# Kernel optimization log

Measured on AMD Instinct MI355X. Metric: run time of the kernel, lower is better.

The kernel has to match this reference:

```python
import jax, jax.numpy as jnp
import numpy as np

D1 = 3          # elevated lattice dim (self.d == self.d1 == 3 in source)
S = 384         # size2d = 128*3
B, N = 32, 65536

# canonical simplex offsets, built exactly as in __init__
_c = np.tile(np.arange(D1), (D1, 1))
for _i in range(1, D1):
    _c[-_i:, _i] = _i - D1
CANONICAL = jnp.asarray(_c, dtype=jnp.int32)  # [[0,1,2],[0,1,-1],[0,-2,-1]]


def setup_inputs() -> dict:
    key = jax.random.key(0)
    k1, k2, k3 = jax.random.split(key, 3)
    # get_model.scalePoints rescales coords to ~0.8*size2d; emulate that range
    pc1 = jax.random.uniform(k1, (B, 3, N), dtype=jnp.float32) * (0.8 * S)
    features = jax.random.normal(k2, (B, 3, N), dtype=jnp.float32)
    tm = jax.random.normal(k3, (B, 3, 3), dtype=jnp.float32)
    # F.normalize(trans_matrix, dim=1)
    trans_mat = tm / jnp.maximum(jnp.linalg.norm(tm, axis=1, keepdims=True), 1e-12)
    return {"pc1": pc1, "features": features, "trans_mat": trans_mat}


def _keys_and_barycentric(pc, trans_mat):
    b, _, n = pc.shape
    elevated = jnp.einsum('bij,bjn->bin', trans_mat, pc)          # (B,3,N)
    greedy = jnp.round(elevated / D1) * D1
    emg = elevated - greedy
    # rank = inverse permutation of descending argsort over the 3 lattice dims
    order = jnp.argsort(-emg, axis=1)
    rank = jnp.argsort(order, axis=1).astype(jnp.int32)           # (B,3,N)
    rs = jnp.sum(greedy, axis=1, keepdims=True) / D1              # (B,1,N)
    rf = rank.astype(jnp.float32)
    cond = (((rf >= D1 - rs) & (rs > 0)) | ((rf < -rs) & (rs < 0))).astype(jnp.float32)
    sign = jnp.where(rs > 0, -1.0, 0.0) + jnp.where(rs < 0, 1.0, 0.0)
    greedy = greedy + D1 * sign * cond
    rank = rank + (D1 * sign * cond).astype(jnp.int32)
    rank = rank + rs.astype(jnp.int32)
    emg2 = elevated - greedy
    greedy_i = greedy.astype(jnp.int32)
    b_ix = jnp.arange(b)[:, None, None]
    n_ix = jnp.arange(n)[None, None, :]
    # NOTE: source uses self.d - rank for += and self.d1 - rank for -=, but d==d1,
    # so the two scatter-adds cancel exactly; barycentric degenerates to [1,0,0].
    # Reproduce the same computation faithfully.
    bary = jnp.zeros((b, D1 + 1, n), jnp.float32)
    bary = bary.at[b_ix, D1 - rank, n_ix].add(emg2)
    bary = bary.at[b_ix, D1 - rank, n_ix].add(-emg2)
    bary = bary / D1
    bary = bary.at[:, 0, :].add(1.0 + bary[:, D1, :])
    bary = bary[:, :D1, :]                                        # (B,3,N)
    keys = greedy_i[:, :, :, None] + CANONICAL[rank]              # (B,3,N,3)
    return keys, bary


def reference(pc1, features, trans_mat):
    keys, bary = _keys_and_barycentric(pc1, trans_mat)
    b = features.shape[0]
    coord = keys[:, :2].reshape(b, 2, -1)                          # (B,2,3N)
    offset = coord.min(axis=2)                                     # (B,2) int
    coord = coord - offset[:, :, None]
    # tmp[b, n*3+j, c] = bary[b, j, n] * features[b, c, n]
    tmp = bary[:, None, :, :] * features[:, :, None, :]            # (B,3,3,N)
    tmp = jnp.transpose(tmp, (0, 1, 3, 2)).reshape(b, 3, -1)       # (B,3,3N)
    tmp = jnp.transpose(tmp, (0, 2, 1))                            # (B,3N,3)
    pts_pick = (-offset) % D1                                      # (B,2)
    oob = coord >= S
    coord = jnp.where(oob, 0, coord)
    bad = jnp.sum(oob, axis=1) > 0                                 # (B,3N)
    tmp = jnp.where(bad[:, :, None], 0.0, tmp)

    ar = jnp.arange(S // D1)

    def splat_one(cd, vals, pick):
        sp = jnp.zeros((S, S, 3), jnp.float32).at[cd[0], cd[1]].add(vals)
        return sp[pick[0] + D1 * ar][:, pick[1] + D1 * ar]

    filter_2d = jax.vmap(splat_one)(coord, tmp, pts_pick)          # (B,S/3,S/3,3)
    return filter_2d
```

## Files before the change

### kernel.cpp

```cpp
#include <hip/hip_runtime.h>
#include <stdint.h>

#define NPTS 65536
#define NB   32
#define SS   384

#define C3INV 0.333333343267440796f

#define FP_SCALE 32768.0f
#define FP_INV   (1.0f / 32768.0f)

__device__ __forceinline__ float fmul_strict(float a, float b) {
    float r;
    asm volatile("v_mul_f32 %0, %1, %2" : "=v"(r) : "v"(a), "v"(b));
    return r;
}
__device__ __forceinline__ float fadd_strict(float a, float b) {
    float r;
    asm volatile("v_add_f32 %0, %1, %2" : "=v"(r) : "v"(a), "v"(b));
    return r;
}

__device__ __forceinline__ void lattice_point(
    const float* __restrict__ t,
    float p0, float p1, float p2,
    int& gi0, int& gi1, int& rc0, int& rc1)
{
    float e0 = fadd_strict(fadd_strict(fmul_strict(t[0], p0), fmul_strict(t[1], p1)), fmul_strict(t[2], p2));
    float e1 = fadd_strict(fadd_strict(fmul_strict(t[3], p0), fmul_strict(t[4], p1)), fmul_strict(t[5], p2));
    float e2 = fadd_strict(fadd_strict(fmul_strict(t[6], p0), fmul_strict(t[7], p1)), fmul_strict(t[8], p2));

    float g0 = __fmul_rn(rintf(__fmul_rn(e0, C3INV)), 3.0f);
    float g1 = __fmul_rn(rintf(__fmul_rn(e1, C3INV)), 3.0f);
    float g2 = __fmul_rn(rintf(__fmul_rn(e2, C3INV)), 3.0f);

    float m0 = e0 - g0, m1 = e1 - g1, m2 = e2 - g2;
    int r0 = (int)(m1 > m0) + (int)(m2 > m0);
    int r1 = (int)(m0 >= m1) + (int)(m2 > m1);

    gi0 = (int)g0;
    gi1 = (int)g1;

    const int irs = (gi0 + gi1 + (int)g2) / 3;

    if (irs > 0) {
        if (r0 >= 3 - irs) { gi0 -= 3; r0 -= 3; }
        if (r1 >= 3 - irs) { gi1 -= 3; r1 -= 3; }
    } else if (irs < 0) {
        if (r0 < -irs) { gi0 += 3; r0 += 3; }
        if (r1 < -irs) { gi1 += 3; r1 += 3; }
    }
    r0 += irs;
    r1 += irs;

    if (r0 < 0) r0 += 3;
    if (r1 < 0) r1 += 3;
    rc0 = min(2, max(0, r0));
    rc1 = min(2, max(0, r1));
}

__device__ __forceinline__ int icl3(int a) {
    return (a >= 0) ? (a + 2) / 3 : -((-a) / 3);
}

__global__ __launch_bounds__(1024) void bin_kernel(
    const float* __restrict__ pc, const float* __restrict__ tmg,
    uint32_t* __restrict__ bins, int* __restrict__ partial)
{
    const int bx  = blockIdx.x;
    const int b   = blockIdx.y;
    const int tid = threadIdx.x;

    __shared__ float t[9];
    if (tid < 9) t[tid] = tmg[b * 9 + tid];
    __syncthreads();

    const float* pcb = pc + (size_t)b * 3 * NPTS;
    const int v = bx * 1024 + tid;

    const float4 P0 = ((const float4*)(pcb + 0 * NPTS))[v];
    const float4 P1 = ((const float4*)(pcb + 1 * NPTS))[v];
    const float4 P2 = ((const float4*)(pcb + 2 * NPTS))[v];

    int km0 = 0x7FFFFFFF, km1 = 0x7FFFFFFF;
    uint32_t pk[4];
    const float p0a[4] = {P0.x, P0.y, P0.z, P0.w};
    const float p1a[4] = {P1.x, P1.y, P1.z, P1.w};
    const float p2a[4] = {P2.x, P2.y, P2.z, P2.w};
#pragma unroll
    for (int i = 0; i < 4; ++i) {
        int gi0, gi1, rc0, rc1;
        lattice_point(t, p0a[i], p1a[i], p2a[i], gi0, gi1, rc0, rc1);
        pk[i] = (uint32_t)(((gi0 / 3 + 512) << 16) | (gi1 / 3 + 512));
        km0 = min(km0, gi0 - rc0);
        km1 = min(km1, gi1 - rc1);
    }
    ((uint4*)(bins + (size_t)b * NPTS))[v] = make_uint4(pk[0], pk[1], pk[2], pk[3]);

#pragma unroll
    for (int off = 32; off > 0; off >>= 1) {
        km0 = min(km0, __shfl_down(km0, off));
        km1 = min(km1, __shfl_down(km1, off));
    }
    __shared__ int s0[16], s1[16];
    if ((tid & 63) == 0) { s0[tid >> 6] = km0; s1[tid >> 6] = km1; }
    __syncthreads();
    if (tid == 0) {
        int m0 = s0[0], m1 = s1[0];
#pragma unroll
        for (int j = 1; j < 16; ++j) { m0 = min(m0, s0[j]); m1 = min(m1, s1[j]); }
        partial[(b * 16 + bx) * 2 + 0] = m0;
        partial[(b * 16 + bx) * 2 + 1] = m1;
    }
}

#define CH_HIST 16384

__global__ __launch_bounds__(1024) void splat_ch_int_kernel(
    const uint32_t* __restrict__ bins, const float* __restrict__ feat,
    const int* __restrict__ partial, int* __restrict__ iout)
{
    const int b     = blockIdx.x;
    const int ch    = blockIdx.y;
    const int chunk = blockIdx.z;
    const int tid   = threadIdx.x;

    __shared__ int ihist[CH_HIST];
#pragma unroll
    for (int i = tid; i < CH_HIST; i += 1024) ihist[i] = 0;

    int off0 = 0x7FFFFFFF, off1 = 0x7FFFFFFF;
#pragma unroll
    for (int j = 0; j < 16; ++j) {
        off0 = min(off0, partial[(b * 16 + j) * 2 + 0]);
        off1 = min(off1, partial[(b * 16 + j) * 2 + 1]);
    }
    __syncthreads();

    const int K0 = 512 + icl3(off0);
    const int K1 = 512 + icl3(off1);

    const uint32_t* bb = bins + (size_t)b * NPTS + (size_t)chunk * (NPTS / 4);
    const float*    fb = feat + ((size_t)b * 3 + ch) * NPTS + (size_t)chunk * (NPTS / 4);

#pragma unroll
    for (int i = 0; i < (NPTS / 4) / 4096; ++i) {
        const int v = i * 1024 + tid;
        const uint4  U = ((const uint4 *)bb)[v];
        const float4 F = ((const float4*)fb)[v];

        const uint32_t ua[4] = {U.x, U.y, U.z, U.w};
        const float    fa[4] = {F.x, F.y, F.z, F.w};

#pragma unroll
        for (int k = 0; k < 4; ++k) {
            const int y = (int)(ua[k] >> 16) - K0;
            const int x = (int)(ua[k] & 0xFFFFu) - K1;
            if (y < 128 && x < 128) {
                const int q = (int)rintf(__fmul_rn(fa[k], FP_SCALE));
                atomicAdd(&ihist[(y << 7) + x], q);
            }
        }
    }
    __syncthreads();

#pragma unroll
    for (int i = tid; i < CH_HIST; i += 1024) {
        const int v = ihist[i];
        if (v != 0) atomicAdd(&iout[(size_t)((b << 14) + i) * 3 + ch], v);
    }
}

__global__ __launch_bounds__(1024) void convert_kernel(float* __restrict__ out)
{
    const int i = blockIdx.x * 1024 + threadIdx.x;
    const int v = ((const int*)out)[i];
    out[i] = __fmul_rn((float)v, FP_INV);
}

#define FTILE_X 16
#define FHIST_F (128 * FTILE_X * 3)

__global__ __launch_bounds__(1024) void kmin2_kernel(
    const float* __restrict__ pc, const float* __restrict__ tmg,
    int* __restrict__ mins)
{
    const int b = blockIdx.y, bx = blockIdx.x, tid = threadIdx.x;
    __shared__ float t[9];
    if (tid < 9) t[tid] = tmg[b * 9 + tid];
    __syncthreads();

    const float* pcb = pc + (size_t)b * 3 * NPTS;
    int km0 = 0x7FFFFFFF, km1 = 0x7FFFFFFF;
    const int n0 = bx * 8192;
#pragma unroll
    for (int i = 0; i < 8; ++i) {
        const int n = n0 + i * 1024 + tid;
        int gi0, gi1, rc0, rc1;
        lattice_point(t, pcb[n], pcb[NPTS + n], pcb[2 * NPTS + n], gi0, gi1, rc0, rc1);
        km0 = min(km0, gi0 - rc0);
        km1 = min(km1, gi1 - rc1);
    }
#pragma unroll
    for (int off = 32; off > 0; off >>= 1) {
        km0 = min(km0, __shfl_down(km0, off));
        km1 = min(km1, __shfl_down(km1, off));
    }
    __shared__ int s0[16], s1[16];
    if ((tid & 63) == 0) { s0[tid >> 6] = km0; s1[tid >> 6] = km1; }
    __syncthreads();
    if (tid == 0) {
        int m0 = s0[0], m1 = s1[0];
#pragma unroll
        for (int j = 1; j < 16; ++j) { m0 = min(m0, s0[j]); m1 = min(m1, s1[j]); }
        atomicMin(&mins[b * 2 + 0], m0);
        atomicMin(&mins[b * 2 + 1], m1);
    }
}

__global__ __launch_bounds__(1024) void splat_recompute_kernel(
    const float* __restrict__ pc, const float* __restrict__ feat,
    const float* __restrict__ tmg, const int* __restrict__ mins,
    float* __restrict__ out)
{
    const int tile = blockIdx.x, b = blockIdx.y, tid = threadIdx.x;
    const int x0 = tile * FTILE_X;

    __shared__ float t[9];
    __shared__ float hist[FHIST_F];
    if (tid < 9) t[tid] = tmg[b * 9 + tid];
#pragma unroll
    for (int i = tid; i < FHIST_F; i += 1024) hist[i] = 0.0f;
    __syncthreads();

    const int off0 = mins[b * 2 + 0];
    const int off1 = mins[b * 2 + 1];
    const float* pcb = pc + (size_t)b * 3 * NPTS;
    const float* ftb = feat + (size_t)b * 3 * NPTS;

    for (int n = tid; n < NPTS; n += 1024) {
        int gi0, gi1, rc0, rc1;
        lattice_point(t, pcb[n], pcb[NPTS + n], pcb[2 * NPTS + n], gi0, gi1, rc0, rc1);
        const int c0 = gi0 - off0;
        const int c1 = gi1 - off1;
        if ((unsigned)c0 < SS && (unsigned)c1 < SS) {
            const int x = c1 / 3;
            if ((x >> 4) == tile) {
                const int y = c0 / 3;
                const int base = (y * FTILE_X + (x - x0)) * 3;
                atomicAdd(&hist[base + 0], ftb[0 * NPTS + n]);
                atomicAdd(&hist[base + 1], ftb[1 * NPTS + n]);
                atomicAdd(&hist[base + 2], ftb[2 * NPTS + n]);
            }
        }
    }
    __syncthreads();
#pragma unroll
    for (int idx = tid; idx < FHIST_F; idx += 1024) {
        const int y   = idx / (FTILE_X * 3);
        const int rem = idx - y * (FTILE_X * 3);
        out[(size_t)(b * 128 + y) * 384 + x0 * 3 + rem] = hist[idx];
    }
}

extern "C" void kernel_launch(void* const* d_in, const int* in_sizes, int n_in,
                              void* d_out, int out_size, void* d_ws, size_t ws_size,
                              hipStream_t stream) {
    const float* pc   = (const float*)d_in[0];
    const float* feat = (const float*)d_in[1];
    const float* tm   = (const float*)d_in[2];
    float* out = (float*)d_out;

    const size_t bins_bytes = (size_t)NB * NPTS * sizeof(uint32_t);
    const size_t need = bins_bytes + 1024 * sizeof(int);

    if (ws_size >= need) {
        uint32_t* bins = (uint32_t*)d_ws;
        int* partial = (int*)((char*)d_ws + bins_bytes);

        hipMemsetAsync(out, 0, (size_t)out_size * sizeof(float), stream);

        dim3 gridA(16, NB);
        bin_kernel<<<gridA, 1024, 0, stream>>>(pc, tm, bins, partial);
        dim3 gridB(NB, 3, 4);
        splat_ch_int_kernel<<<gridB, 1024, 0, stream>>>(bins, feat, partial, (int*)out);
        convert_kernel<<<(out_size + 1023) / 1024, 1024, 0, stream>>>(out);
    } else {
        int* mins = (int*)d_ws;
        hipMemsetAsync(mins, 0x7F, 64 * sizeof(int), stream);
        dim3 grid(8, NB);
        kmin2_kernel<<<grid, 1024, 0, stream>>>(pc, tm, mins);
        dim3 gridB2(8, NB);
        splat_recompute_kernel<<<gridB2, 1024, 0, stream>>>(pc, feat, tm, mins, out);
    }
}
```

Before: 123.3 us.

## Stage per-chunk histograms in workspace and reduce deterministically instead of global atomics

Each splat block now writes its full 128x128 integer histogram to a staging buffer with vectorized stores, replacing sparse global atomicAdds into the output. A new sum_convert kernel adds the four chunk partials per channel, converts to float and writes the interleaved output directly. This removes the output memset, the global atomics and the separate convert pass. In exchange it writes and reads about 25 MB of staging traffic and needs a larger workspace, falling back to the old path when the workspace is too small.

```diff
diff --git a/kernel.cpp b/kernel.cpp
--- a/kernel.cpp
+++ b/kernel.cpp
@@ -116,18 +116,19 @@
 
 #define CH_HIST 16384
 
-__global__ __launch_bounds__(1024) void splat_ch_int_kernel(
+__global__ __launch_bounds__(1024) void splat_ch_stage_kernel(
     const uint32_t* __restrict__ bins, const float* __restrict__ feat,
-    const int* __restrict__ partial, int* __restrict__ iout)
+    const int* __restrict__ partial, int* __restrict__ stg)
 {
     const int b     = blockIdx.x;
     const int ch    = blockIdx.y;
     const int chunk = blockIdx.z;
     const int tid   = threadIdx.x;
 
-    __shared__ int ihist[CH_HIST];
-#pragma unroll
-    for (int i = tid; i < CH_HIST; i += 1024) ihist[i] = 0;
+    __shared__ __align__(16) int ihist[CH_HIST];
+#pragma unroll
+    for (int j = 0; j < 4; ++j)
+        ((int4*)ihist)[j * 1024 + tid] = make_int4(0, 0, 0, 0);
 
     int off0 = 0x7FFFFFFF, off1 = 0x7FFFFFFF;
 #pragma unroll
@@ -152,6 +153,88 @@
         const uint32_t ua[4] = {U.x, U.y, U.z, U.w};
         const float    fa[4] = {F.x, F.y, F.z, F.w};
 
+#pragma unroll
+        for (int k = 0; k < 4; ++k) {
+            const int y = (int)(ua[k] >> 16) - K0;
+            const int x = (int)(ua[k] & 0xFFFFu) - K1;
+            if (y < 128 && x < 128) {
+                const int q = (int)rintf(__fmul_rn(fa[k], FP_SCALE));
+                atomicAdd(&ihist[(y << 7) + x], q);
+            }
+        }
+    }
+    __syncthreads();
+
+    int4* dst = (int4*)(stg + (size_t)(((b * 3 + ch) << 2) + chunk) * CH_HIST);
+#pragma unroll
+    for (int j = 0; j < 4; ++j)
+        dst[j * 1024 + tid] = ((const int4*)ihist)[j * 1024 + tid];
+}
+
+__global__ __launch_bounds__(1024) void sum_convert_kernel(
+    const int* __restrict__ stg, float* __restrict__ out)
+{
+    const int t = blockIdx.x * 1024 + threadIdx.x;
+    const int b = blockIdx.y;
+
+    float o[12];
+#pragma unroll
+    for (int ch = 0; ch < 3; ++ch) {
+        const int4* s = (const int4*)(stg + (size_t)((b * 3 + ch) << 2) * CH_HIST);
+        const int4 a0 = s[t];
+        const int4 a1 = s[t + 1 * (CH_HIST / 4)];
+        const int4 a2 = s[t + 2 * (CH_HIST / 4)];
+        const int4 a3 = s[t + 3 * (CH_HIST / 4)];
+        const int vx = a0.x + a1.x + a2.x + a3.x;
+        const int vy = a0.y + a1.y + a2.y + a3.y;
+        const int vz = a0.z + a1.z + a2.z + a3.z;
+        const int vw = a0.w + a1.w + a2.w + a3.w;
+        o[0 * 3 + ch] = __fmul_rn((float)vx, FP_INV);
+        o[1 * 3 + ch] = __fmul_rn((float)vy, FP_INV);
+        o[2 * 3 + ch] = __fmul_rn((float)vz, FP_INV);
+        o[3 * 3 + ch] = __fmul_rn((float)vw, FP_INV);
+    }
+
+    float4* op = (float4*)(out + ((size_t)((b << 14) + t * 4)) * 3);
+    op[0] = make_float4(o[0], o[1],  o[2],  o[3]);
+    op[1] = make_float4(o[4], o[5],  o[6],  o[7]);
+    op[2] = make_float4(o[8], o[9],  o[10], o[11]);
+}
+
+__global__ __launch_bounds__(1024) void splat_ch_int_kernel(
+    const uint32_t* __restrict__ bins, const float* __restrict__ feat,
+    const int* __restrict__ partial, int* __restrict__ iout)
+{
+    const int b     = blockIdx.x;
+    const int ch    = blockIdx.y;
+    const int chunk = blockIdx.z;
+    const int tid   = threadIdx.x;
+
+    __shared__ int ihist[CH_HIST];
+#pragma unroll
+    for (int i = tid; i < CH_HIST; i += 1024) ihist[i] = 0;
+
+    int off0 = 0x7FFFFFFF, off1 = 0x7FFFFFFF;
+#pragma unroll
+    for (int j = 0; j < 16; ++j) {
+        off0 = min(off0, partial[(b * 16 + j) * 2 + 0]);
+        off1 = min(off1, partial[(b * 16 + j) * 2 + 1]);
+    }
+    __syncthreads();
+
+    const int K0 = 512 + icl3(off0);
+    const int K1 = 512 + icl3(off1);
+
+    const uint32_t* bb = bins + (size_t)b * NPTS + (size_t)chunk * (NPTS / 4);
+    const float*    fb = feat + ((size_t)b * 3 + ch) * NPTS + (size_t)chunk * (NPTS / 4);
+
+#pragma unroll
+    for (int i = 0; i < (NPTS / 4) / 4096; ++i) {
+        const int v = i * 1024 + tid;
+        const uint4  U = ((const uint4 *)bb)[v];
+        const float4 F = ((const float4*)fb)[v];
+        const uint32_t ua[4] = {U.x, U.y, U.z, U.w};
+        const float    fa[4] = {F.x, F.y, F.z, F.w};
 #pragma unroll
         for (int k = 0; k < 4; ++k) {
             const int y = (int)(ua[k] >> 16) - K0;
@@ -272,9 +355,21 @@
     float* out = (float*)d_out;
 
     const size_t bins_bytes = (size_t)NB * NPTS * sizeof(uint32_t);
-    const size_t need = bins_bytes + 1024 * sizeof(int);
-
-    if (ws_size >= need) {
+    const size_t part_bytes = 1024 * sizeof(int);
+    const size_t stg_bytes  = (size_t)NB * 3 * 4 * CH_HIST * sizeof(int);
+
+    if (ws_size >= bins_bytes + part_bytes + stg_bytes) {
+        uint32_t* bins = (uint32_t*)d_ws;
+        int* partial = (int*)((char*)d_ws + bins_bytes);
+        int* stg     = (int*)((char*)d_ws + bins_bytes + part_bytes);
+
+        dim3 gridA(16, NB);
+        bin_kernel<<<gridA, 1024, 0, stream>>>(pc, tm, bins, partial);
+        dim3 gridB(NB, 3, 4);
+        splat_ch_stage_kernel<<<gridB, 1024, 0, stream>>>(bins, feat, partial, stg);
+        dim3 gridC(4, NB);
+        sum_convert_kernel<<<gridC, 1024, 0, stream>>>(stg, out);
+    } else if (ws_size >= bins_bytes + part_bytes) {
         uint32_t* bins = (uint32_t*)d_ws;
         int* partial = (int*)((char*)d_ws + bins_bytes);
 
```

Measured after the change: 102.0 us. 17.3% less time.

## Split splat histogram by output row strips to drop memset and convert passes

Applied to the files above, without the earlier changes.

The splat kernel now partitions output rows into 8 strips of 16 rows. Each block scans all points of a batch and channel but accumulates only into its own strip, so it owns that output region outright. It writes float results directly, which removes the output memset, the global atomics and the separate int-to-float convert kernel. In exchange every block rereads the full bins and features arrays, eight times the global read traffic of the old chunked split, and it uses smaller 512-thread blocks.

```diff
diff --git a/kernel.cpp b/kernel.cpp
--- a/kernel.cpp
+++ b/kernel.cpp
@@ -63,6 +63,7 @@
     return (a >= 0) ? (a + 2) / 3 : -((-a) / 3);
 }
 
+
 __global__ __launch_bounds__(1024) void bin_kernel(
     const float* __restrict__ pc, const float* __restrict__ tmg,
     uint32_t* __restrict__ bins, int* __restrict__ partial)
@@ -114,20 +115,22 @@
     }
 }
 
-#define CH_HIST 16384
-
-__global__ __launch_bounds__(1024) void splat_ch_int_kernel(
+#define NSTRIP     8
+#define STRIP_ROWS 16
+#define STRIP_INTS (STRIP_ROWS * 128)
+#define STHREADS   512
+
+__global__ __launch_bounds__(STHREADS) void splat_strip_kernel(
     const uint32_t* __restrict__ bins, const float* __restrict__ feat,
-    const int* __restrict__ partial, int* __restrict__ iout)
+    const int* __restrict__ partial, float* __restrict__ out)
 {
     const int b     = blockIdx.x;
     const int ch    = blockIdx.y;
-    const int chunk = blockIdx.z;
+    const int strip = blockIdx.z;
     const int tid   = threadIdx.x;
 
-    __shared__ int ihist[CH_HIST];
-#pragma unroll
-    for (int i = tid; i < CH_HIST; i += 1024) ihist[i] = 0;
+    __shared__ __align__(16) int ihist[STRIP_INTS];
+    ((int4*)ihist)[tid] = make_int4(0, 0, 0, 0);
 
     int off0 = 0x7FFFFFFF, off1 = 0x7FFFFFFF;
 #pragma unroll
@@ -137,15 +140,15 @@
     }
     __syncthreads();
 
-    const int K0 = 512 + icl3(off0);
+    const int K0 = 512 + icl3(off0) + strip * STRIP_ROWS;
     const int K1 = 512 + icl3(off1);
 
-    const uint32_t* bb = bins + (size_t)b * NPTS + (size_t)chunk * (NPTS / 4);
-    const float*    fb = feat + ((size_t)b * 3 + ch) * NPTS + (size_t)chunk * (NPTS / 4);
-
-#pragma unroll
-    for (int i = 0; i < (NPTS / 4) / 4096; ++i) {
-        const int v = i * 1024 + tid;
+    const uint32_t* bb = bins + (size_t)b * NPTS;
+    const float*    fb = feat + ((size_t)b * 3 + ch) * NPTS;
+
+#pragma unroll 4
+    for (int i = 0; i < (NPTS / 4) / STHREADS; ++i) {
+        const int v = i * STHREADS + tid;
         const uint4  U = ((const uint4 *)bb)[v];
         const float4 F = ((const float4*)fb)[v];
 
@@ -156,7 +159,7 @@
         for (int k = 0; k < 4; ++k) {
             const int y = (int)(ua[k] >> 16) - K0;
             const int x = (int)(ua[k] & 0xFFFFu) - K1;
-            if (y < 128 && x < 128) {
+            if ((unsigned)y < STRIP_ROWS && (unsigned)x < 128u) {
                 const int q = (int)rintf(__fmul_rn(fa[k], FP_SCALE));
                 atomicAdd(&ihist[(y << 7) + x], q);
             }
@@ -165,17 +168,12 @@
     __syncthreads();
 
 #pragma unroll
-    for (int i = tid; i < CH_HIST; i += 1024) {
-        const int v = ihist[i];
-        if (v != 0) atomicAdd(&iout[(size_t)((b << 14) + i) * 3 + ch], v);
-    }
-}
-
-__global__ __launch_bounds__(1024) void convert_kernel(float* __restrict__ out)
-{
-    const int i = blockIdx.x * 1024 + threadIdx.x;
-    const int v = ((const int*)out)[i];
-    out[i] = __fmul_rn((float)v, FP_INV);
+    for (int j = 0; j < STRIP_INTS / STHREADS; ++j) {
+        const int idx = j * STHREADS + tid;
+        const int v = ihist[idx];
+        out[((size_t)(b << 14) + (size_t)strip * STRIP_INTS + idx) * 3 + ch] =
+            __fmul_rn((float)v, FP_INV);
+    }
 }
 
 #define FTILE_X 16
@@ -272,19 +270,17 @@
     float* out = (float*)d_out;
 
     const size_t bins_bytes = (size_t)NB * NPTS * sizeof(uint32_t);
-    const size_t need = bins_bytes + 1024 * sizeof(int);
+    const size_t part_bytes = 4096;
+    const size_t need = bins_bytes + part_bytes;
 
     if (ws_size >= need) {
         uint32_t* bins = (uint32_t*)d_ws;
         int* partial = (int*)((char*)d_ws + bins_bytes);
 
-        hipMemsetAsync(out, 0, (size_t)out_size * sizeof(float), stream);
-
         dim3 gridA(16, NB);
         bin_kernel<<<gridA, 1024, 0, stream>>>(pc, tm, bins, partial);
-        dim3 gridB(NB, 3, 4);
-        splat_ch_int_kernel<<<gridB, 1024, 0, stream>>>(bins, feat, partial, (int*)out);
-        convert_kernel<<<(out_size + 1023) / 1024, 1024, 0, stream>>>(out);
+        dim3 gridB(NB, 3, NSTRIP);
+        splat_strip_kernel<<<gridB, STHREADS, 0, stream>>>(bins, feat, partial, out);
     } else {
         int* mins = (int*)d_ws;
         hipMemsetAsync(mins, 0x7F, 64 * sizeof(int), stream);
```

Measured after the change: 112.7 us. 8.6% less time.
